# Optimization experiments

Hardware: AMD Instinct MI355X
Metric: run time of the kernel (lower is better)

The kernel has to match this reference:

```python
import jax, jax.numpy as jnp
import numpy as np

B, S, D, H = 2, 2048, 1024, 16
HD = D // H
EPS = 1e-8


def setup_inputs() -> dict:
    key = jax.random.key(0)
    ks = jax.random.split(key, 6)
    x = jax.random.normal(ks[0], (B, S, D), jnp.float32)
    V = jax.random.normal(ks[1], (B, S, H, HD), jnp.float32)
    # binary sparsity mask [B, S, S]
    M = (jax.random.uniform(ks[2], (B, S, S)) > 0.5).astype(jnp.float32)
    # packed QKV in-projection of nn.MultiheadAttention
    in_proj_w = jax.random.normal(ks[3], (3 * D, D), jnp.float32) / np.sqrt(D).astype(np.float32)
    in_proj_b = jnp.zeros((3 * D,), jnp.float32)
    # module-level out_proj (the mha's internal out_proj is discarded)
    out_w = jax.random.normal(ks[4], (D, D), jnp.float32) / np.sqrt(D).astype(np.float32)
    out_b = jnp.zeros((D,), jnp.float32)
    return dict(x=x, V=V, M=M, in_proj_w=in_proj_w, in_proj_b=in_proj_b,
                out_w=out_w, out_b=out_b)


def reference(x, V, M, in_proj_w, in_proj_b, out_w, out_b):
    b, s, d = x.shape
    # packed QKV projection (torch MHA semantics); v-proj computed but its
    # output path (mha output) is discarded by the module, so skip it.
    qkv = x @ in_proj_w.T + in_proj_b              # [B,S,3D]
    q, k, _ = jnp.split(qkv, 3, axis=-1)
    q = q.reshape(b, s, H, HD).transpose(0, 2, 1, 3)   # [B,H,S,HD]
    k = k.reshape(b, s, H, HD).transpose(0, 2, 1, 3)
    scale = np.float32(1.0 / np.sqrt(HD))
    scores = jnp.einsum('bhsd,bhtd->bhst', q, k) * scale  # [B,H,S,S]
    A = jax.nn.softmax(scores, axis=-1)
    # mask + L1 renormalization over keys
    A_sparse = A * M[:, None, :, :]
    norm = jnp.sum(jnp.abs(A_sparse), axis=-1, keepdims=True) + EPS
    A_bar = A_sparse / norm
    # separate value tensor V: [B,S,H,HD] -> [B,H,S,HD]
    Vp = V.transpose(0, 2, 1, 3)
    out = jnp.einsum('bhst,bhtd->bhsd', A_bar, Vp)  # [B,H,S,HD]
    out = out.transpose(0, 2, 1, 3).reshape(b, s, d)
    return out @ out_w.T + out_b
```

## Files before the change

### kernel.cpp

```cpp
#include <hip/hip_runtime.h>
#include <hip/hip_bf16.h>

#define B_  2
#define S_  2048
#define D_  1024
#define H_  16
#define HD_ 64

using bf16x8  = __attribute__((ext_vector_type(8))) __bf16;
using floatx4 = __attribute__((ext_vector_type(4))) float;
using intx4   = __attribute__((ext_vector_type(4))) int;

__device__ __forceinline__ float bf2f(unsigned short u) {
  union { unsigned int i; float f; } v; v.i = ((unsigned int)u) << 16; return v.f;
}
__device__ __forceinline__ unsigned short f2bf(float f) {
  union { float f; unsigned int i; } v; v.f = f;
  unsigned int r = v.i + 0x7fffu + ((v.i >> 16) & 1u);
  return (unsigned short)(r >> 16);
}
__device__ __forceinline__ floatx4 mfma16(bf16x8 a, bf16x8 b, floatx4 c) {
  return __builtin_amdgcn_mfma_f32_16x16x32_bf16(a, b, c, 0, 0, 0);
}
__device__ __forceinline__ void gld16(const unsigned short* g, unsigned short* l) {
  __builtin_amdgcn_global_load_lds(
      (const __attribute__((address_space(1))) unsigned int*)g,
      (__attribute__((address_space(3))) unsigned int*)l, 16, 0, 0);
}
#define SW8(row, g) ((((g) ^ ((row) & 7)) * 8))
#define SW4(row, g) ((((g) ^ (((row) >> 1) & 3)) * 8))

__global__ __launch_bounds__(256) void cvt_f32_bf16(
    const float* __restrict__ in, unsigned short* __restrict__ out, int n)
{
  const int i = (blockIdx.x * 256 + threadIdx.x) * 8;
  if (i + 8 > n) return;
  float4 a = *(const float4*)(in + i);
  float4 b = *(const float4*)(in + i + 4);
  union { unsigned short u[8]; intx4 v; } p;
  p.u[0] = f2bf(a.x); p.u[1] = f2bf(a.y); p.u[2] = f2bf(a.z); p.u[3] = f2bf(a.w);
  p.u[4] = f2bf(b.x); p.u[5] = f2bf(b.y); p.u[6] = f2bf(b.z); p.u[7] = f2bf(b.w);
  *(intx4*)(out + i) = p.v;
}

__global__ __launch_bounds__(256) void pack_mask(
    const float* __restrict__ M, unsigned long long* __restrict__ out)
{
  const int word = blockIdx.x * 4 + (threadIdx.x >> 6);
  const int lane = threadIdx.x & 63;
  float v = M[(size_t)word * 64 + lane];
  unsigned long long b = __ballot(v != 0.0f);
  if (lane == 0) out[word] = b;
}

__global__ __launch_bounds__(256) void gemm_abt(
    const unsigned short* __restrict__ A,
    const unsigned short* __restrict__ Bm,
    const float* __restrict__ bias,
    unsigned short* __restrict__ Cb, float* __restrict__ Cf,
    int M, int N, int K, int qscale)
{
  __shared__ unsigned short As[128 * 32];
  __shared__ unsigned short Bs[128 * 32];

  const int tid  = threadIdx.x;
  const int wave = tid >> 6, lane = tid & 63;
  const int quad = lane >> 4, l15 = lane & 15;
  const int wr = wave >> 1, wc = wave & 1;
  const int bm = blockIdx.y * 128, bn = blockIdx.x * 128;
  const int srow = tid >> 2, gs = tid & 3;

  floatx4 acc[4][4];
#pragma unroll
  for (int mt = 0; mt < 4; ++mt)
#pragma unroll
    for (int nt = 0; nt < 4; ++nt)
      acc[mt][nt] = (floatx4){0.f, 0.f, 0.f, 0.f};

  for (int k0 = 0; k0 < K; k0 += 32) {
    __syncthreads();
#pragma unroll
    for (int r = 0; r < 2; ++r) {
      const int row = srow + r * 64;
      gld16(&A[(size_t)(bm + row) * K + k0 + SW4(row, gs)],
            &As[wave * 512 + r * 2048]);
      gld16(&Bm[(size_t)(bn + row) * K + k0 + SW4(row, gs)],
            &Bs[wave * 512 + r * 2048]);
    }
    __syncthreads();

    bf16x8 af[4], bf[4];
#pragma unroll
    for (int mt = 0; mt < 4; ++mt) {
      const int row = wr * 64 + mt * 16 + l15;
      af[mt] = *(const bf16x8*)&As[row * 32 + SW4(row, quad)];
    }
#pragma unroll
    for (int nt = 0; nt < 4; ++nt) {
      const int row = wc * 64 + nt * 16 + l15;
      bf[nt] = *(const bf16x8*)&Bs[row * 32 + SW4(row, quad)];
    }
#pragma unroll
    for (int mt = 0; mt < 4; ++mt)
#pragma unroll
      for (int nt = 0; nt < 4; ++nt)
        acc[mt][nt] = mfma16(af[mt], bf[nt], acc[mt][nt]);
  }

#pragma unroll
  for (int nt = 0; nt < 4; ++nt) {
    const int col = bn + wc * 64 + nt * 16 + l15;
    const float bi = bias[col];
    const float sc = (qscale && col < 1024) ? 0.125f : 1.0f;
#pragma unroll
    for (int mt = 0; mt < 4; ++mt) {
      const int row0 = bm + wr * 64 + mt * 16 + quad * 4;
#pragma unroll
      for (int reg = 0; reg < 4; ++reg) {
        const float v = (acc[mt][nt][reg] + bi) * sc;
        if (Cf) Cf[(size_t)(row0 + reg) * N + col] = v;
        else    Cb[(size_t)(row0 + reg) * N + col] = f2bf(v);
      }
    }
  }
}

__global__ __launch_bounds__(256) void transpose_v(
    const float* __restrict__ V, unsigned short* __restrict__ Vt)
{
  __shared__ unsigned short tile[64 * 72];
  const int tid = threadIdx.x;
  const int b = blockIdx.z, h = blockIdx.y, t0 = blockIdx.x * 64;
  const int sr = tid >> 3, sc = (tid & 7) * 8;

  const float* src = V + ((size_t)((b * S_ + t0) * H_ + h)) * HD_;
#pragma unroll
  for (int half = 0; half < 2; ++half) {
    const int r = sr + half * 32;
    float4 v0 = *(const float4*)&src[(size_t)r * (H_ * HD_) + sc];
    float4 v1 = *(const float4*)&src[(size_t)r * (H_ * HD_) + sc + 4];
    union { unsigned short u[8]; intx4 v; } p;
    p.u[0] = f2bf(v0.x); p.u[1] = f2bf(v0.y); p.u[2] = f2bf(v0.z); p.u[3] = f2bf(v0.w);
    p.u[4] = f2bf(v1.x); p.u[5] = f2bf(v1.y); p.u[6] = f2bf(v1.z); p.u[7] = f2bf(v1.w);
    *(intx4*)&tile[r * 72 + sc] = p.v;
  }
  __syncthreads();

  unsigned short* dst = Vt + ((size_t)((b * H_ + h) * HD_)) * S_ + t0;
  union { unsigned short u[8]; intx4 v; } pack;
#pragma unroll
  for (int j = 0; j < 8; ++j) pack.u[j] = tile[(sc + j) * 72 + sr];
  *(intx4*)&dst[(size_t)sr * S_ + sc] = pack.v;
#pragma unroll
  for (int j = 0; j < 8; ++j) pack.u[j] = tile[(sc + j) * 72 + sr + 32];
  *(intx4*)&dst[(size_t)(sr + 32) * S_ + sc] = pack.v;
}

__global__ __launch_bounds__(256) void attn_kernel(
    const unsigned short* __restrict__ QK,
    const unsigned short* __restrict__ Vt,
    const unsigned long long* __restrict__ Mpk,
    unsigned short* __restrict__ ctx)
{
  __shared__ unsigned short Qs[128 * 64];
  __shared__ unsigned short Ks[64 * 64];
  __shared__ unsigned short Vs[64 * 64];
  __shared__ unsigned short Ps[128 * 72];
  __shared__ unsigned long long Ms64[128];

  const int tid  = threadIdx.x;
  const int wave = tid >> 6, lane = tid & 63;
  const int quad = lane >> 4, l15 = lane & 15;
  const int b = blockIdx.z, h = blockIdx.y, qb = blockIdx.x * 128;
  const int gs = tid & 7;

  const unsigned short* Qbase = QK + (size_t)(b * S_ + qb) * 2048 + h * HD_;
  const unsigned short* Kbase = QK + (size_t)(b * S_) * 2048 + D_ + h * HD_;
  const unsigned short* Vbase = Vt + (size_t)((b * H_ + h) * HD_) * S_;

#pragma unroll
  for (int r = 0; r < 4; ++r) {
    const int row = (tid >> 3) + r * 32;
    gld16(Qbase + (size_t)row * 2048 + SW8(row, gs), &Qs[wave * 512 + r * 2048]);
  }
  __syncthreads();

  bf16x8 qf[2][2];
#pragma unroll
  for (int mt = 0; mt < 2; ++mt)
#pragma unroll
    for (int c = 0; c < 2; ++c) {
      const int row = wave * 32 + mt * 16 + l15;
      qf[mt][c] = *(const bf16x8*)&Qs[row * 64 + SW8(row, c * 4 + quad)];
    }

  floatx4 accO[2][4];
  float Pp[2][4];
#pragma unroll
  for (int mt = 0; mt < 2; ++mt)
#pragma unroll
    for (int nt = 0; nt < 4; ++nt) {
      accO[mt][nt] = (floatx4){0.f, 0.f, 0.f, 0.f};
      Pp[mt][nt] = 0.f;
    }

  for (int t0 = 0; t0 < S_; t0 += 64) {
    __syncthreads();
#pragma unroll
    for (int r = 0; r < 2; ++r) {
      const int row = (tid >> 3) + r * 32;
      gld16(Kbase + (size_t)(t0 + row) * 2048 + SW8(row, gs),
            &Ks[wave * 512 + r * 2048]);
      gld16(Vbase + (size_t)row * S_ + t0 + SW8(row, gs),
            &Vs[wave * 512 + r * 2048]);
    }
    if (tid < 128)
      Ms64[tid] = Mpk[(size_t)(b * S_ + qb + tid) * (S_ / 64) + (t0 >> 6)];
    __syncthreads();

    floatx4 sc[2][4];
#pragma unroll
    for (int nt = 0; nt < 4; ++nt) {
      bf16x8 kf0, kf1;
      {
        const int row = nt * 16 + l15;
        kf0 = *(const bf16x8*)&Ks[row * 64 + SW8(row, quad)];
        kf1 = *(const bf16x8*)&Ks[row * 64 + SW8(row, 4 + quad)];
      }
#pragma unroll
      for (int mt = 0; mt < 2; ++mt) {
        floatx4 z = (floatx4){0.f, 0.f, 0.f, 0.f};
        z = mfma16(qf[mt][0], kf0, z);
        z = mfma16(qf[mt][1], kf1, z);
        sc[mt][nt] = z;
      }
    }

    unsigned long long mw[2][4];
#pragma unroll
    for (int mt = 0; mt < 2; ++mt)
#pragma unroll
      for (int reg = 0; reg < 4; ++reg)
        mw[mt][reg] = Ms64[wave * 32 + mt * 16 + quad * 4 + reg];

#pragma unroll
    for (int mt = 0; mt < 2; ++mt)
#pragma unroll
      for (int nt = 0; nt < 4; ++nt) {
#pragma unroll
        for (int reg = 0; reg < 4; ++reg) {
          float e = __expf(sc[mt][nt][reg]);
          unsigned int w32 = (nt < 2) ? (unsigned int)mw[mt][reg]
                                      : (unsigned int)(mw[mt][reg] >> 32);
          float p = ((w32 >> ((nt & 1) * 16 + l15)) & 1u) ? e : 0.0f;
          Pp[mt][reg] += p;
          const int row = wave * 32 + mt * 16 + quad * 4 + reg;
          Ps[row * 72 + SW8(row, nt * 2 + (l15 >> 3)) + (l15 & 7)] = f2bf(p);
        }
      }

    __syncthreads();

#pragma unroll
    for (int nt = 0; nt < 4; ++nt) {
      bf16x8 vf0, vf1;
      {
        const int row = nt * 16 + l15;
        vf0 = *(const bf16x8*)&Vs[row * 64 + SW8(row, quad)];
        vf1 = *(const bf16x8*)&Vs[row * 64 + SW8(row, 4 + quad)];
      }
#pragma unroll
      for (int mt = 0; mt < 2; ++mt) {
        const int row = wave * 32 + mt * 16 + l15;
        bf16x8 pf0 = *(const bf16x8*)&Ps[row * 72 + SW8(row, quad)];
        bf16x8 pf1 = *(const bf16x8*)&Ps[row * 72 + SW8(row, 4 + quad)];
        accO[mt][nt] = mfma16(pf0, vf0, accO[mt][nt]);
        accO[mt][nt] = mfma16(pf1, vf1, accO[mt][nt]);
      }
    }
  }

#pragma unroll
  for (int off = 1; off <= 8; off <<= 1)
#pragma unroll
    for (int mt = 0; mt < 2; ++mt)
#pragma unroll
      for (int reg = 0; reg < 4; ++reg)
        Pp[mt][reg] += __shfl_xor(Pp[mt][reg], off);

#pragma unroll
  for (int mt = 0; mt < 2; ++mt)
#pragma unroll
    for (int reg = 0; reg < 4; ++reg)
      Pp[mt][reg] = 1.0f / (Pp[mt][reg] + 1e-30f);

#pragma unroll
  for (int mt = 0; mt < 2; ++mt)
#pragma unroll
    for (int nt = 0; nt < 4; ++nt)
#pragma unroll
      for (int reg = 0; reg < 4; ++reg) {
        const int row = wave * 32 + mt * 16 + quad * 4 + reg;
        ctx[(size_t)(b * S_ + qb + row) * D_ + h * HD_ + nt * 16 + l15] =
            f2bf(accO[mt][nt][reg] * Pp[mt][reg]);
      }
}

extern "C" void kernel_launch(void* const* d_in, const int* in_sizes, int n_in,
                              void* d_out, int out_size, void* d_ws, size_t ws_size,
                              hipStream_t stream) {
  const float* x     = (const float*)d_in[0];
  const float* V     = (const float*)d_in[1];
  const float* Mm    = (const float*)d_in[2];
  const float* w_in  = (const float*)d_in[3];
  const float* b_in  = (const float*)d_in[4];
  const float* w_out = (const float*)d_in[5];
  const float* b_out = (const float*)d_in[6];
  float* out = (float*)d_out;

  unsigned short* qk  = (unsigned short*)d_ws;
  unsigned short* vt  = qk  + (size_t)8 * 1024 * 1024;
  unsigned short* ctx = vt  + (size_t)4 * 1024 * 1024;
  unsigned short* xb  = ctx + (size_t)4 * 1024 * 1024;
  unsigned short* wb  = xb  + (size_t)4 * 1024 * 1024;
  unsigned short* wob = wb  + (size_t)2 * 1024 * 1024;
  unsigned long long* mpk = (unsigned long long*)(wob + (size_t)1024 * 1024);

  const int nX  = B_ * S_ * D_;
  const int nW  = 2 * D_ * D_;
  const int nWo = D_ * D_;
  const int nWords = B_ * S_ * (S_ / 64);

  cvt_f32_bf16<<<nX  / 2048, 256, 0, stream>>>(x,     xb,  nX);
  cvt_f32_bf16<<<nW  / 2048, 256, 0, stream>>>(w_in,  wb,  nW);
  cvt_f32_bf16<<<nWo / 2048, 256, 0, stream>>>(w_out, wob, nWo);
  pack_mask<<<nWords / 4, 256, 0, stream>>>(Mm, mpk);

  gemm_abt<<<dim3(2048 / 128, (B_ * S_) / 128), 256, 0, stream>>>(
      xb, wb, b_in, qk, nullptr, B_ * S_, 2048, D_, 1);

  transpose_v<<<dim3(S_ / 64, H_, B_), 256, 0, stream>>>(V, vt);

  attn_kernel<<<dim3(S_ / 128, H_, B_), 256, 0, stream>>>(qk, vt, mpk, ctx);

  gemm_abt<<<dim3(D_ / 128, (B_ * S_) / 128), 256, 0, stream>>>(
      ctx, wob, b_out, nullptr, out, B_ * S_, D_, D_, 0);
}
```

Baseline: 272.1 us.

## Fuse prep kernels into one launch and double-buffer K/V tiles in attention

Merges the three fp32-to-bf16 conversions, mask packing and V transpose into a single prep kernel dispatched by block index, which removes four kernel launches. The attention kernel now double-buffers K, V and mask tiles so the next tile's global-to-LDS loads overlap the current tile's compute. It also reuses the Q staging buffer for P and drops one barrier per iteration, relying on manual waitcnt. Conversions use packed bf16 intrinsics. Removing the barrier between the P writes and the P reads depends on each wave reading only its own rows, which is fragile, and the double buffers increase LDS use.

```diff
diff --git a/kernel.cpp b/kernel.cpp
--- a/kernel.cpp
+++ b/kernel.cpp
@@ -19,6 +19,11 @@
   unsigned int r = v.i + 0x7fffu + ((v.i >> 16) & 1u);
   return (unsigned short)(r >> 16);
 }
+__device__ __forceinline__ unsigned int f2bf_pk(float a, float b) {
+  union { __hip_bfloat162 h2; unsigned int u; } c;
+  c.h2 = __float22bfloat162_rn(make_float2(a, b));
+  return c.u;
+}
 __device__ __forceinline__ floatx4 mfma16(bf16x8 a, bf16x8 b, floatx4 c) {
   return __builtin_amdgcn_mfma_f32_16x16x32_bf16(a, b, c, 0, 0, 0);
 }
@@ -30,27 +35,63 @@
 #define SW8(row, g) ((((g) ^ ((row) & 7)) * 8))
 #define SW4(row, g) ((((g) ^ (((row) >> 1) & 3)) * 8))
 
-__global__ __launch_bounds__(256) void cvt_f32_bf16(
-    const float* __restrict__ in, unsigned short* __restrict__ out, int n)
+__global__ __launch_bounds__(256) void prep_kernel(
+    const float* __restrict__ x, const float* __restrict__ w_in,
+    const float* __restrict__ w_out, const float* __restrict__ V,
+    const float* __restrict__ Mm,
+    unsigned short* __restrict__ xb, unsigned short* __restrict__ wb,
+    unsigned short* __restrict__ wob, unsigned short* __restrict__ vt,
+    unsigned long long* __restrict__ mpk)
 {
-  const int i = (blockIdx.x * 256 + threadIdx.x) * 8;
-  if (i + 8 > n) return;
-  float4 a = *(const float4*)(in + i);
-  float4 b = *(const float4*)(in + i + 4);
-  union { unsigned short u[8]; intx4 v; } p;
-  p.u[0] = f2bf(a.x); p.u[1] = f2bf(a.y); p.u[2] = f2bf(a.z); p.u[3] = f2bf(a.w);
-  p.u[4] = f2bf(b.x); p.u[5] = f2bf(b.y); p.u[6] = f2bf(b.z); p.u[7] = f2bf(b.w);
-  *(intx4*)(out + i) = p.v;
-}
-
-__global__ __launch_bounds__(256) void pack_mask(
-    const float* __restrict__ M, unsigned long long* __restrict__ out)
-{
-  const int word = blockIdx.x * 4 + (threadIdx.x >> 6);
-  const int lane = threadIdx.x & 63;
-  float v = M[(size_t)word * 64 + lane];
-  unsigned long long b = __ballot(v != 0.0f);
-  if (lane == 0) out[word] = b;
+  __shared__ unsigned short tile[64 * 72];
+  const int bid = blockIdx.x, tid = threadIdx.x;
+
+  if (bid < 3584) {
+    const float* src; unsigned short* dst; int base;
+    if (bid < 2048)      { src = x;     dst = xb;  base = bid; }
+    else if (bid < 3072) { src = w_in;  dst = wb;  base = bid - 2048; }
+    else                 { src = w_out; dst = wob; base = bid - 3072; }
+    const int i = (base * 256 + tid) * 8;
+    float4 a = *(const float4*)(src + i);
+    float4 b = *(const float4*)(src + i + 4);
+    union { unsigned int w[4]; intx4 v; } o;
+    o.w[0] = f2bf_pk(a.x, a.y); o.w[1] = f2bf_pk(a.z, a.w);
+    o.w[2] = f2bf_pk(b.x, b.y); o.w[3] = f2bf_pk(b.z, b.w);
+    *(intx4*)(dst + i) = o.v;
+  } else if (bid < 5632) {
+    const int wave = tid >> 6, lane = tid & 63;
+    const int w0 = (bid - 3584) * 64 + wave * 16;
+#pragma unroll 4
+    for (int j = 0; j < 16; ++j) {
+      float v = Mm[(size_t)(w0 + j) * 64 + lane];
+      unsigned long long bl = __ballot(v != 0.0f);
+      if (lane == 0) mpk[w0 + j] = bl;
+    }
+  } else {
+    const int idx = bid - 5632;
+    const int t0 = (idx & 31) * 64, h = (idx >> 5) & 15, b = idx >> 9;
+    const int sr = tid >> 3, sc = (tid & 7) * 8;
+    const float* src = V + ((size_t)((b * S_ + t0) * H_ + h)) * HD_;
+#pragma unroll
+    for (int half = 0; half < 2; ++half) {
+      const int r = sr + half * 32;
+      float4 v0 = *(const float4*)&src[(size_t)r * (H_ * HD_) + sc];
+      float4 v1 = *(const float4*)&src[(size_t)r * (H_ * HD_) + sc + 4];
+      union { unsigned int w[4]; intx4 v; } p;
+      p.w[0] = f2bf_pk(v0.x, v0.y); p.w[1] = f2bf_pk(v0.z, v0.w);
+      p.w[2] = f2bf_pk(v1.x, v1.y); p.w[3] = f2bf_pk(v1.z, v1.w);
+      *(intx4*)&tile[r * 72 + sc] = p.v;
+    }
+    __syncthreads();
+    unsigned short* dst = vt + ((size_t)((b * H_ + h) * HD_)) * S_ + t0;
+    union { unsigned short u[8]; intx4 v; } pack;
+#pragma unroll
+    for (int j = 0; j < 8; ++j) pack.u[j] = tile[(sc + j) * 72 + sr];
+    *(intx4*)&dst[(size_t)sr * S_ + sc] = pack.v;
+#pragma unroll
+    for (int j = 0; j < 8; ++j) pack.u[j] = tile[(sc + j) * 72 + sr + 32];
+    *(intx4*)&dst[(size_t)(sr + 32) * S_ + sc] = pack.v;
+  }
 }
 
 __global__ __launch_bounds__(256) void gemm_abt(
@@ -125,48 +166,16 @@
   }
 }
 
-__global__ __launch_bounds__(256) void transpose_v(
-    const float* __restrict__ V, unsigned short* __restrict__ Vt)
-{
-  __shared__ unsigned short tile[64 * 72];
-  const int tid = threadIdx.x;
-  const int b = blockIdx.z, h = blockIdx.y, t0 = blockIdx.x * 64;
-  const int sr = tid >> 3, sc = (tid & 7) * 8;
-
-  const float* src = V + ((size_t)((b * S_ + t0) * H_ + h)) * HD_;
-#pragma unroll
-  for (int half = 0; half < 2; ++half) {
-    const int r = sr + half * 32;
-    float4 v0 = *(const float4*)&src[(size_t)r * (H_ * HD_) + sc];
-    float4 v1 = *(const float4*)&src[(size_t)r * (H_ * HD_) + sc + 4];
-    union { unsigned short u[8]; intx4 v; } p;
-    p.u[0] = f2bf(v0.x); p.u[1] = f2bf(v0.y); p.u[2] = f2bf(v0.z); p.u[3] = f2bf(v0.w);
-    p.u[4] = f2bf(v1.x); p.u[5] = f2bf(v1.y); p.u[6] = f2bf(v1.z); p.u[7] = f2bf(v1.w);
-    *(intx4*)&tile[r * 72 + sc] = p.v;
-  }
-  __syncthreads();
-
-  unsigned short* dst = Vt + ((size_t)((b * H_ + h) * HD_)) * S_ + t0;
-  union { unsigned short u[8]; intx4 v; } pack;
-#pragma unroll
-  for (int j = 0; j < 8; ++j) pack.u[j] = tile[(sc + j) * 72 + sr];
-  *(intx4*)&dst[(size_t)sr * S_ + sc] = pack.v;
-#pragma unroll
-  for (int j = 0; j < 8; ++j) pack.u[j] = tile[(sc + j) * 72 + sr + 32];
-  *(intx4*)&dst[(size_t)(sr + 32) * S_ + sc] = pack.v;
-}
-
 __global__ __launch_bounds__(256) void attn_kernel(
     const unsigned short* __restrict__ QK,
     const unsigned short* __restrict__ Vt,
     const unsigned long long* __restrict__ Mpk,
     unsigned short* __restrict__ ctx)
 {
-  __shared__ unsigned short Qs[128 * 64];
-  __shared__ unsigned short Ks[64 * 64];
-  __shared__ unsigned short Vs[64 * 64];
-  __shared__ unsigned short Ps[128 * 72];
-  __shared__ unsigned long long Ms64[128];
+  __shared__ unsigned short PQ[128 * 72];
+  __shared__ unsigned short Ks[2][64 * 64];
+  __shared__ unsigned short Vs[2][64 * 64];
+  __shared__ unsigned long long Ms64[2][128];
 
   const int tid  = threadIdx.x;
   const int wave = tid >> 6, lane = tid & 63;
@@ -177,12 +186,21 @@
   const unsigned short* Qbase = QK + (size_t)(b * S_ + qb) * 2048 + h * HD_;
   const unsigned short* Kbase = QK + (size_t)(b * S_) * 2048 + D_ + h * HD_;
   const unsigned short* Vbase = Vt + (size_t)((b * H_ + h) * HD_) * S_;
+  const unsigned long long* Mbase = Mpk + (size_t)(b * S_ + qb) * (S_ / 64);
 
 #pragma unroll
   for (int r = 0; r < 4; ++r) {
     const int row = (tid >> 3) + r * 32;
-    gld16(Qbase + (size_t)row * 2048 + SW8(row, gs), &Qs[wave * 512 + r * 2048]);
-  }
+    gld16(Qbase + (size_t)row * 2048 + SW8(row, gs), &PQ[wave * 512 + r * 2048]);
+  }
+#pragma unroll
+  for (int r = 0; r < 2; ++r) {
+    const int row = (tid >> 3) + r * 32;
+    gld16(Kbase + (size_t)row * 2048 + SW8(row, gs), &Ks[0][wave * 512 + r * 2048]);
+    gld16(Vbase + (size_t)row * S_ + SW8(row, gs),   &Vs[0][wave * 512 + r * 2048]);
+  }
+  if (tid < 128) Ms64[0][tid] = Mbase[(size_t)tid * (S_ / 64)];
+  asm volatile("s_waitcnt vmcnt(0)" ::: "memory");
   __syncthreads();
 
   bf16x8 qf[2][2];
@@ -191,8 +209,9 @@
 #pragma unroll
     for (int c = 0; c < 2; ++c) {
       const int row = wave * 32 + mt * 16 + l15;
-      qf[mt][c] = *(const bf16x8*)&Qs[row * 64 + SW8(row, c * 4 + quad)];
-    }
+      qf[mt][c] = *(const bf16x8*)&PQ[row * 64 + SW8(row, c * 4 + quad)];
+    }
+  asm volatile("s_waitcnt lgkmcnt(0)" ::: "memory");
 
   floatx4 accO[2][4];
   float Pp[2][4];
@@ -204,29 +223,31 @@
       Pp[mt][nt] = 0.f;
     }
 
-  for (int t0 = 0; t0 < S_; t0 += 64) {
+  for (int i = 0; i < 32; ++i) {
+    const int cur = i & 1, nxt = cur ^ 1;
+    asm volatile("s_waitcnt vmcnt(0)" ::: "memory");
     __syncthreads();
-#pragma unroll
-    for (int r = 0; r < 2; ++r) {
-      const int row = (tid >> 3) + r * 32;
-      gld16(Kbase + (size_t)(t0 + row) * 2048 + SW8(row, gs),
-            &Ks[wave * 512 + r * 2048]);
-      gld16(Vbase + (size_t)row * S_ + t0 + SW8(row, gs),
-            &Vs[wave * 512 + r * 2048]);
-    }
-    if (tid < 128)
-      Ms64[tid] = Mpk[(size_t)(b * S_ + qb + tid) * (S_ / 64) + (t0 >> 6)];
-    __syncthreads();
+
+    if (i + 1 < 32) {
+      const int t1 = (i + 1) * 64;
+#pragma unroll
+      for (int r = 0; r < 2; ++r) {
+        const int row = (tid >> 3) + r * 32;
+        gld16(Kbase + (size_t)(t1 + row) * 2048 + SW8(row, gs),
+              &Ks[nxt][wave * 512 + r * 2048]);
+        gld16(Vbase + (size_t)row * S_ + t1 + SW8(row, gs),
+              &Vs[nxt][wave * 512 + r * 2048]);
+      }
+      if (tid < 128)
+        Ms64[nxt][tid] = Mbase[(size_t)tid * (S_ / 64) + i + 1];
+    }
 
     floatx4 sc[2][4];
 #pragma unroll
     for (int nt = 0; nt < 4; ++nt) {
-      bf16x8 kf0, kf1;
-      {
-        const int row = nt * 16 + l15;
-        kf0 = *(const bf16x8*)&Ks[row * 64 + SW8(row, quad)];
-        kf1 = *(const bf16x8*)&Ks[row * 64 + SW8(row, 4 + quad)];
-      }
+      const int row = nt * 16 + l15;
+      bf16x8 kf0 = *(const bf16x8*)&Ks[cur][row * 64 + SW8(row, quad)];
+      bf16x8 kf1 = *(const bf16x8*)&Ks[cur][row * 64 + SW8(row, 4 + quad)];
 #pragma unroll
       for (int mt = 0; mt < 2; ++mt) {
         floatx4 z = (floatx4){0.f, 0.f, 0.f, 0.f};
@@ -241,41 +262,51 @@
     for (int mt = 0; mt < 2; ++mt)
 #pragma unroll
       for (int reg = 0; reg < 4; ++reg)
-        mw[mt][reg] = Ms64[wave * 32 + mt * 16 + quad * 4 + reg];
+        mw[mt][reg] = Ms64[cur][wave * 32 + mt * 16 + quad * 4 + reg];
 
 #pragma unroll
     for (int mt = 0; mt < 2; ++mt)
 #pragma unroll
-      for (int nt = 0; nt < 4; ++nt) {
-#pragma unroll
-        for (int reg = 0; reg < 4; ++reg) {
-          float e = __expf(sc[mt][nt][reg]);
-          unsigned int w32 = (nt < 2) ? (unsigned int)mw[mt][reg]
-                                      : (unsigned int)(mw[mt][reg] >> 32);
-          float p = ((w32 >> ((nt & 1) * 16 + l15)) & 1u) ? e : 0.0f;
-          Pp[mt][reg] += p;
-          const int row = wave * 32 + mt * 16 + quad * 4 + reg;
-          Ps[row * 72 + SW8(row, nt * 2 + (l15 >> 3)) + (l15 & 7)] = f2bf(p);
+      for (int nt = 0; nt < 4; ++nt)
+#pragma unroll
+        for (int rp = 0; rp < 2; ++rp) {
+          const int r0 = rp * 2, r1 = rp * 2 + 1;
+          float e0 = __expf(sc[mt][nt][r0]);
+          float e1 = __expf(sc[mt][nt][r1]);
+          unsigned int w0 = (nt < 2) ? (unsigned int)mw[mt][r0]
+                                     : (unsigned int)(mw[mt][r0] >> 32);
+          unsigned int w1 = (nt < 2) ? (unsigned int)mw[mt][r1]
+                                     : (unsigned int)(mw[mt][r1] >> 32);
+          const int sh = (nt & 1) * 16 + l15;
+          float p0 = ((w0 >> sh) & 1u) ? e0 : 0.0f;
+          float p1 = ((w1 >> sh) & 1u) ? e1 : 0.0f;
+          Pp[mt][r0] += p0;
+          Pp[mt][r1] += p1;
+          unsigned int u = f2bf_pk(p0, p1);
+          const int rowA = wave * 32 + mt * 16 + quad * 4 + r0;
+          const int cg = nt * 2 + (l15 >> 3), co = l15 & 7;
+          PQ[rowA * 72 + SW8(rowA, cg) + co] = (unsigned short)u;
+          PQ[(rowA + 1) * 72 + SW8(rowA + 1, cg) + co] = (unsigned short)(u >> 16);
         }
-      }
-
-    __syncthreads();
-
+
+    asm volatile("s_waitcnt lgkmcnt(0)" ::: "memory");
+
+    bf16x8 pf0[2], pf1[2];
+#pragma unroll
+    for (int mt = 0; mt < 2; ++mt) {
+      const int row = wave * 32 + mt * 16 + l15;
+      pf0[mt] = *(const bf16x8*)&PQ[row * 72 + SW8(row, quad)];
+      pf1[mt] = *(const bf16x8*)&PQ[row * 72 + SW8(row, 4 + quad)];
+    }
 #pragma unroll
     for (int nt = 0; nt < 4; ++nt) {
-      bf16x8 vf0, vf1;
-      {
-        const int row = nt * 16 + l15;
-        vf0 = *(const bf16x8*)&Vs[row * 64 + SW8(row, quad)];
-        vf1 = *(const bf16x8*)&Vs[row * 64 + SW8(row, 4 + quad)];
-      }
+      const int row = nt * 16 + l15;
+      bf16x8 vf0 = *(const bf16x8*)&Vs[cur][row * 64 + SW8(row, quad)];
+      bf16x8 vf1 = *(const bf16x8*)&Vs[cur][row * 64 + SW8(row, 4 + quad)];
 #pragma unroll
       for (int mt = 0; mt < 2; ++mt) {
-        const int row = wave * 32 + mt * 16 + l15;
-        bf16x8 pf0 = *(const bf16x8*)&Ps[row * 72 + SW8(row, quad)];
-        bf16x8 pf1 = *(const bf16x8*)&Ps[row * 72 + SW8(row, 4 + quad)];
-        accO[mt][nt] = mfma16(pf0, vf0, accO[mt][nt]);
-        accO[mt][nt] = mfma16(pf1, vf1, accO[mt][nt]);
+        accO[mt][nt] = mfma16(pf0[mt], vf0, accO[mt][nt]);
+        accO[mt][nt] = mfma16(pf1[mt], vf1, accO[mt][nt]);
       }
     }
   }
@@ -326,21 +357,12 @@
   unsigned short* wob = wb  + (size_t)2 * 1024 * 1024;
   unsigned long long* mpk = (unsigned long long*)(wob + (size_t)1024 * 1024);
 
-  const int nX  = B_ * S_ * D_;
-  const int nW  = 2 * D_ * D_;
-  const int nWo = D_ * D_;
-  const int nWords = B_ * S_ * (S_ / 64);
-
-  cvt_f32_bf16<<<nX  / 2048, 256, 0, stream>>>(x,     xb,  nX);
-  cvt_f32_bf16<<<nW  / 2048, 256, 0, stream>>>(w_in,  wb,  nW);
-  cvt_f32_bf16<<<nWo / 2048, 256, 0, stream>>>(w_out, wob, nWo);
-  pack_mask<<<nWords / 4, 256, 0, stream>>>(Mm, mpk);
+  prep_kernel<<<6656, 256, 0, stream>>>(x, w_in, w_out, V, Mm,
+                                        xb, wb, wob, vt, mpk);
 
   gemm_abt<<<dim3(2048 / 128, (B_ * S_) / 128), 256, 0, stream>>>(
       xb, wb, b_in, qk, nullptr, B_ * S_, 2048, D_, 1);
 
-  transpose_v<<<dim3(S_ / 64, H_, B_), 256, 0, stream>>>(V, vt);
-
   attn_kernel<<<dim3(S_ / 128, H_, B_), 256, 0, stream>>>(qk, vt, mpk, ctx);
 
   gemm_abt<<<dim3(D_ / 128, (B_ * S_) / 128), 256, 0, stream>>>(
```

Measured after the change: 258.4 us. 1.05x faster.
